# Optimization experiments

Measured on AMD Instinct MI355X. Metric: run time of the kernel, lower is better.

The kernel has to match this reference:

```python
import jax, jax.numpy as jnp
import numpy as np

TAU_FILTER_INV = 1000.0
DT = 0.001
# decay = 1 - alpha = exp(-dt * tau_filter_inv)
DECAY = float(np.exp(-DT * TAU_FILTER_INV))


def setup_inputs() -> dict:
    key = jax.random.key(0)
    k1, k2, k3 = jax.random.split(key, 3)
    T, B, I, O = 2048, 32, 256, 256
    input_tensor = jax.random.normal(k1, (T, B, I), dtype=jnp.float32)
    # Linear weight init mimics uniform(-k, k), k = sqrt(1/input_size)
    k = float(np.sqrt(1.0 / I))
    W = jax.random.uniform(k2, (O, I), dtype=jnp.float32, minval=-k, maxval=k)
    b = jax.random.uniform(k3, (O,), dtype=jnp.float32, minval=-k, maxval=k)
    return {"input_tensor": input_tensor, "W": W, "b": b}


def reference(input_tensor, W, b):
    # Dense projection: [T, B, I] @ [I, O] -> [T, B, O]
    y = jnp.einsum("tbi,oi->tbo", input_tensor, W) + b
    decay = jnp.asarray(DECAY, dtype=y.dtype)

    # s(t) = y(t) + decay * s(t-1); s(0) = y(0) (init state 0)
    def step(s, x):
        s = x + decay * s
        return s, s

    _, out = jax.lax.scan(step, jnp.zeros_like(y[0]), y)
    return out
```

## Files before the change

kernel.cpp:

```cpp
#include <hip/hip_runtime.h>
#include <cstddef>


#define DECAY  0.36787944117144233f
#define D8     0.00033546262790251185f
#define INV1MD 1.5819767068693265f

typedef __attribute__((ext_vector_type(8))) short short8;
typedef __attribute__((ext_vector_type(4))) short short4v;
typedef __attribute__((ext_vector_type(4))) float f32x4;

static constexpr int T_DIM = 2048, B_DIM = 32, K_DIM = 256, N_DIM = 256;
static constexpr int M_DIM = T_DIM * B_DIM;
static constexpr int PS  = 32768;
static constexpr int TCH = 64;

__device__ __forceinline__ float bfbits2f(unsigned short u) {
  unsigned int x = ((unsigned int)u) << 16;
  return __builtin_bit_cast(float, x);
}
__device__ __forceinline__ short f2bf_s(float f) {
  __bf16 h = (__bf16)f;
  return __builtin_bit_cast(short, h);
}

__global__ void k_split_w(const float* __restrict__ W, short* __restrict__ Wh) {
  const int o = blockIdx.x, i = threadIdx.x;
  size_t off = (size_t)(o >> 7) * PS + (i >> 5) * 4096 + ((i >> 3) & 3) * 1024 +
               (o & 127) * 8 + (i & 7);
  Wh[off] = f2bf_s(W[o * 256 + i]);
}

__global__ __launch_bounds__(512, 4)
void k_fused(const float* __restrict__ X, const short* __restrict__ Wth,
             const float* __restrict__ bias, float* __restrict__ out) {
  __shared__ __align__(16) char ldsA[65536];
  __shared__ __align__(16) float cb[8 * 256];
  __shared__ float cfac[TCH];

  const int tid  = threadIdx.x;
  const int lane = tid & 63;
  const int wv   = tid >> 6;
  const int c    = blockIdx.x;
  const int b    = blockIdx.y;
  const int t0   = c * TCH;

  if (tid < TCH)
    cfac[tid] = (1.f - __expf(-(float)(t0 + tid + 1))) * INV1MD;

  const int ch4 = lane * 4;
  const float* xp = X + (size_t)(t0 + wv * 8) * 8192 + b * 256 + ch4;
  const bool warm = (wv == 0) && (c > 0);

  f32x4 xw[8];
  if (warm) {
    const float* wp = xp - (size_t)8 * 8192;
    #pragma unroll
    for (int j = 0; j < 8; ++j)
      xw[j] = *reinterpret_cast<const f32x4*>(wp + (size_t)j * 8192);
  }
  f32x4 xr[8];
  #pragma unroll
  for (int j = 0; j < 8; ++j)
    xr[j] = *reinterpret_cast<const f32x4*>(xp + (size_t)j * 8192);

  f32x4 s = {0.f, 0.f, 0.f, 0.f};
  if (warm) {
    #pragma unroll
    for (int j = 0; j < 8; ++j) s = xw[j] + s * DECAY;
  }
  f32x4 y[8];
  #pragma unroll
  for (int j = 0; j < 8; ++j) { s = xr[j] + s * DECAY; y[j] = s; }

  *reinterpret_cast<f32x4*>(&cb[wv * 256 + ch4]) = s;

  const int row16 = lane & 15;
  const int kq    = lane >> 4;
  const int rg    = wv >> 2;
  const int cg    = wv & 3;
  const short* Whp = Wth + (size_t)(cg >> 1) * PS;
  const int wbase  = kq * 1024 + (((cg & 1) * 64) + row16) * 8;

  short8 bh[2][4];
  #pragma unroll
  for (int ct = 0; ct < 4; ++ct)
    bh[0][ct] = *reinterpret_cast<const short8*>(Whp + wbase + ct * 128);
  __builtin_amdgcn_sched_barrier(0);

  __syncthreads();

  f32x4 cin = {0.f, 0.f, 0.f, 0.f};
  {
    float m = 1.f;
    for (int v = wv - 1; v >= 0; --v) {
      f32x4 cv = *reinterpret_cast<const f32x4*>(&cb[v * 256 + ch4]);
      cin = cin + cv * m;
      m *= D8;
    }
  }

  static const float DP[8] = {0.36787944f, 0.13533528f, 0.049787067f,
                              0.018315639f, 0.0067379470f, 0.0024787522f,
                              0.00091188197f, 0.00033546263f};
  #pragma unroll
  for (int j = 0; j < 8; ++j) {
    f32x4 yy = y[j] + cin * DP[j];
    const int row = wv * 8 + j;
    short4v hv, lv;
    #pragma unroll
    for (int e = 0; e < 4; ++e) {
      short h = f2bf_s(yy[e]);
      hv[e] = h;
      lv[e] = f2bf_s(yy[e] - bfbits2f((unsigned short)h));
    }
    const int byte = (row * 512 + ch4 * 2) ^ ((row & 7) << 4);
    *reinterpret_cast<short4v*>(ldsA + byte)         = hv;
    *reinterpret_cast<short4v*>(ldsA + 32768 + byte) = lv;
  }
  __syncthreads();

  f32x4 acc[2][4] = {};
  #pragma unroll
  for (int kt = 0; kt < 8; ++kt) {
    const int cur = kt & 1;
    if (kt < 7) {
      #pragma unroll
      for (int ct = 0; ct < 4; ++ct)
        bh[cur ^ 1][ct] = *reinterpret_cast<const short8*>(
            Whp + (kt + 1) * 4096 + wbase + ct * 128);
      __builtin_amdgcn_sched_barrier(0);
    }
    short8 ah[2], al[2];
    #pragma unroll
    for (int rt = 0; rt < 2; ++rt) {
      const int row = rg * 32 + rt * 16 + row16;
      const int byte = (row * 512 + kt * 64 + kq * 16) ^ ((row & 7) << 4);
      ah[rt] = *reinterpret_cast<const short8*>(ldsA + byte);
      al[rt] = *reinterpret_cast<const short8*>(ldsA + 32768 + byte);
    }
    #pragma unroll
    for (int rt = 0; rt < 2; ++rt)
      #pragma unroll
      for (int ct = 0; ct < 4; ++ct) {
        acc[rt][ct] = __builtin_amdgcn_mfma_f32_16x16x32_bf16(ah[rt], bh[cur][ct], acc[rt][ct], 0, 0, 0);
        acc[rt][ct] = __builtin_amdgcn_mfma_f32_16x16x32_bf16(al[rt], bh[cur][ct], acc[rt][ct], 0, 0, 0);
      }
  }

  __syncthreads();
  #pragma unroll
  for (int rt = 0; rt < 2; ++rt)
    #pragma unroll
    for (int ct = 0; ct < 4; ++ct)
      #pragma unroll
      for (int j = 0; j < 4; ++j) {
        const int row = rg * 32 + rt * 16 + kq * 4 + j;
        const int col = cg * 64 + ct * 16 + row16;
        const int byte = (row * 1024 + col * 4) ^ ((row & 7) << 4);
        *reinterpret_cast<float*>(ldsA + byte) = acc[rt][ct][j];
      }
  __syncthreads();
  const f32x4* bias4 = reinterpret_cast<const f32x4*>(bias);
  #pragma unroll
  for (int j = 0; j < 8; ++j) {
    const int idx  = tid + j * 512;
    const int row  = idx >> 6;
    const int colc = idx & 63;
    const int byte = (idx * 16) ^ ((row & 7) << 4);
    f32x4 yv = *reinterpret_cast<const f32x4*>(ldsA + byte);
    f32x4 bv = bias4[colc];
    const float cf = cfac[row];
    f32x4 r;
    #pragma unroll
    for (int e = 0; e < 4; ++e) r[e] = fmaf(bv[e], cf, yv[e]);
    *reinterpret_cast<f32x4*>(out + ((size_t)(t0 + row) * 32 + b) * 256 +
                              colc * 4) = r;
  }
}

__global__ void k_fb_gemm(const float* __restrict__ X, const float* __restrict__ W,
                          const float* __restrict__ bias, float* __restrict__ Y) {
  size_t idx = (size_t)blockIdx.x * 256 + threadIdx.x;
  int o = (int)(idx & 255);
  size_t m = idx >> 8;
  const float* x = X + m * 256;
  const float* w = W + (size_t)o * 256;
  float s = bias[o];
  for (int k = 0; k < 256; ++k) s = fmaf(x[k], w[k], s);
  Y[idx] = s;
}
__global__ void k_fb_scan(float* __restrict__ Y) {
  int ch = blockIdx.x * 256 + threadIdx.x;
  float s = 0.f;
  float* p = Y + ch;
  for (int t = 0; t < 2048; ++t) { s = fmaf(DECAY, s, *p); *p = s; p += 8192; }
}

extern "C" void kernel_launch(void* const* d_in, const int* in_sizes, int n_in,
                              void* d_out, int out_size, void* d_ws, size_t ws_size,
                              hipStream_t stream) {
  const float* X    = (const float*)d_in[0];
  const float* W    = (const float*)d_in[1];
  const float* bias = (const float*)d_in[2];
  float* out = (float*)d_out;

  const size_t w_elems = (size_t)N_DIM * K_DIM;
  const size_t need    = w_elems * sizeof(short);

  if (ws_size >= need) {
    short* Wh = (short*)d_ws;
    k_split_w<<<N_DIM, 256, 0, stream>>>(W, Wh);
    k_fused<<<dim3(T_DIM / TCH, B_DIM), 512, 0, stream>>>(X, Wh, bias, out);
  } else {
    k_fb_gemm<<<M_DIM, 256, 0, stream>>>(X, W, bias, out);
    k_fb_scan<<<32, 256, 0, stream>>>(out);
  }
}
```

Before: 39.72 us.

## Drop split-bf16 low part, halve LDS, overlap scan chunks for higher occupancy

Replaces the hi+lo bf16 split of the scanned activations with a single bf16 operand, which halves the MFMA count and the A-tile LDS. The scan is restructured so each wave covers 9 overlapping timesteps, removing the separate warm-up pass, and the carry buffer is stored as bf16. LDS shrinks enough to raise launch bounds to 6 blocks per CU. The GEMM is re-tiled so each wave owns 32 output columns across all 64 rows, and the epilogue is staged in two halves. Dropping the low part reduces accuracy of the projection, which may exceed tolerance.

```diff
diff --git a/kernel.cpp b/kernel.cpp
--- a/kernel.cpp
+++ b/kernel.cpp
@@ -3,7 +3,7 @@
 
 
 #define DECAY  0.36787944117144233f
-#define D8     0.00033546262790251185f
+#define D9     1.2340980408667956e-4f
 #define INV1MD 1.5819767068693265f
 
 typedef __attribute__((ext_vector_type(8))) short short8;
@@ -31,11 +31,11 @@
   Wh[off] = f2bf_s(W[o * 256 + i]);
 }
 
-__global__ __launch_bounds__(512, 4)
+__global__ __launch_bounds__(512, 6)
 void k_fused(const float* __restrict__ X, const short* __restrict__ Wth,
              const float* __restrict__ bias, float* __restrict__ out) {
-  __shared__ __align__(16) char ldsA[65536];
-  __shared__ __align__(16) float cb[8 * 256];
+  __shared__ __align__(16) char ldsA[32768];
+  __shared__ __align__(16) short cbh[8 * 256];
   __shared__ float cfac[TCH];
 
   const int tid  = threadIdx.x;
@@ -44,138 +44,158 @@
   const int c    = blockIdx.x;
   const int b    = blockIdx.y;
   const int t0   = c * TCH;
+  const int ch4  = lane * 4;
+
+  const int row16 = lane & 15;
+  const int kq    = lane >> 4;
+  const int cg    = wv;
+  const short* Wp = Wth + (size_t)(cg >> 2) * PS;
+  const int wr0   = (cg & 3) * 32;
+
+  short8 bh[2][2][2];
+  #pragma unroll
+  for (int ki = 0; ki < 2; ++ki)
+    #pragma unroll
+    for (int ct = 0; ct < 2; ++ct)
+      bh[0][ki][ct] = *reinterpret_cast<const short8*>(
+          Wp + ki * 4096 + kq * 1024 + (wr0 + ct * 16 + row16) * 8);
+  __builtin_amdgcn_sched_barrier(0);
 
   if (tid < TCH)
     cfac[tid] = (1.f - __expf(-(float)(t0 + tid + 1))) * INV1MD;
 
-  const int ch4 = lane * 4;
-  const float* xp = X + (size_t)(t0 + wv * 8) * 8192 + b * 256 + ch4;
-  const bool warm = (wv == 0) && (c > 0);
-
-  f32x4 xw[8];
-  if (warm) {
-    const float* wp = xp - (size_t)8 * 8192;
-    #pragma unroll
-    for (int j = 0; j < 8; ++j)
-      xw[j] = *reinterpret_cast<const f32x4*>(wp + (size_t)j * 8192);
-  }
-  f32x4 xr[8];
-  #pragma unroll
-  for (int j = 0; j < 8; ++j)
-    xr[j] = *reinterpret_cast<const f32x4*>(xp + (size_t)j * 8192);
-
-  f32x4 s = {0.f, 0.f, 0.f, 0.f};
-  if (warm) {
-    #pragma unroll
-    for (int j = 0; j < 8; ++j) s = xw[j] + s * DECAY;
-  }
-  f32x4 y[8];
-  #pragma unroll
-  for (int j = 0; j < 8; ++j) { s = xr[j] + s * DECAY; y[j] = s; }
-
-  *reinterpret_cast<f32x4*>(&cb[wv * 256 + ch4]) = s;
-
-  const int row16 = lane & 15;
-  const int kq    = lane >> 4;
-  const int rg    = wv >> 2;
-  const int cg    = wv & 3;
-  const short* Whp = Wth + (size_t)(cg >> 1) * PS;
-  const int wbase  = kq * 1024 + (((cg & 1) * 64) + row16) * 8;
-
-  short8 bh[2][4];
-  #pragma unroll
-  for (int ct = 0; ct < 4; ++ct)
-    bh[0][ct] = *reinterpret_cast<const short8*>(Whp + wbase + ct * 128);
-  __builtin_amdgcn_sched_barrier(0);
-
+  f32x4 y[9];
+  {
+    const int ts = t0 + wv * 9 - 8;
+    if (ts >= 0) {
+      const float* xp = X + (size_t)ts * 8192 + b * 256 + ch4;
+      f32x4 xr[9];
+      #pragma unroll
+      for (int j = 0; j < 9; ++j)
+        xr[j] = *reinterpret_cast<const f32x4*>(xp + (size_t)j * 8192);
+      f32x4 s = {0.f, 0.f, 0.f, 0.f};
+      #pragma unroll
+      for (int j = 0; j < 9; ++j) {
+        #pragma unroll
+        for (int e = 0; e < 4; ++e) s[e] = fmaf(DECAY, s[e], xr[j][e]);
+        y[j] = s;
+      }
+    } else {
+      y[8] = *reinterpret_cast<const f32x4*>(X + b * 256 + ch4);
+    }
+  }
+  {
+    short4v cv;
+    #pragma unroll
+    for (int e = 0; e < 4; ++e) cv[e] = f2bf_s(y[8][e]);
+    *reinterpret_cast<short4v*>(&cbh[wv * 256 + ch4]) = cv;
+  }
   __syncthreads();
 
   f32x4 cin = {0.f, 0.f, 0.f, 0.f};
   {
     float m = 1.f;
     for (int v = wv - 1; v >= 0; --v) {
-      f32x4 cv = *reinterpret_cast<const f32x4*>(&cb[v * 256 + ch4]);
-      cin = cin + cv * m;
-      m *= D8;
-    }
-  }
-
-  static const float DP[8] = {0.36787944f, 0.13533528f, 0.049787067f,
-                              0.018315639f, 0.0067379470f, 0.0024787522f,
-                              0.00091188197f, 0.00033546263f};
-  #pragma unroll
-  for (int j = 0; j < 8; ++j) {
-    f32x4 yy = y[j] + cin * DP[j];
-    const int row = wv * 8 + j;
-    short4v hv, lv;
-    #pragma unroll
-    for (int e = 0; e < 4; ++e) {
-      short h = f2bf_s(yy[e]);
-      hv[e] = h;
-      lv[e] = f2bf_s(yy[e] - bfbits2f((unsigned short)h));
-    }
-    const int byte = (row * 512 + ch4 * 2) ^ ((row & 7) << 4);
-    *reinterpret_cast<short4v*>(ldsA + byte)         = hv;
-    *reinterpret_cast<short4v*>(ldsA + 32768 + byte) = lv;
+      short4v cv = *reinterpret_cast<const short4v*>(&cbh[v * 256 + ch4]);
+      #pragma unroll
+      for (int e = 0; e < 4; ++e)
+        cin[e] = fmaf(bfbits2f((unsigned short)cv[e]), m, cin[e]);
+      m *= D9;
+    }
+  }
+
+  {
+    static constexpr float DP[9] = {
+        0.36787944117144233f, 0.1353352832366127f,  0.049787068367863944f,
+        0.018315638888734179f, 0.006737946999085467f, 0.0024787521766663585f,
+        0.0009118819655545162f, 0.00033546262790251185f, 1.2340980408667956e-4f};
+    #pragma unroll
+    for (int j = 0; j < 9; ++j) {
+      const int r = wv * 9 + j - 8;
+      if (r >= 0) {
+        short4v hv;
+        #pragma unroll
+        for (int e = 0; e < 4; ++e)
+          hv[e] = f2bf_s(fmaf(cin[e], DP[j], y[j][e]));
+        const int byte = (r * 512 + ch4 * 2) ^ ((r & 7) << 4);
+        *reinterpret_cast<short4v*>(ldsA + byte) = hv;
+      }
+    }
   }
   __syncthreads();
 
-  f32x4 acc[2][4] = {};
-  #pragma unroll
-  for (int kt = 0; kt < 8; ++kt) {
-    const int cur = kt & 1;
-    if (kt < 7) {
-      #pragma unroll
-      for (int ct = 0; ct < 4; ++ct)
-        bh[cur ^ 1][ct] = *reinterpret_cast<const short8*>(
-            Whp + (kt + 1) * 4096 + wbase + ct * 128);
+  #pragma unroll
+  for (int ki = 0; ki < 2; ++ki)
+    #pragma unroll
+    for (int ct = 0; ct < 2; ++ct)
+      bh[1][ki][ct] = *reinterpret_cast<const short8*>(
+          Wp + (2 + ki) * 4096 + kq * 1024 + (wr0 + ct * 16 + row16) * 8);
+  __builtin_amdgcn_sched_barrier(0);
+
+  f32x4 acc[4][2] = {};
+  #pragma unroll
+  for (int g = 0; g < 4; ++g) {
+    #pragma unroll
+    for (int ki = 0; ki < 2; ++ki) {
+      const int kt = g * 2 + ki;
+      short8 ah[4];
+      #pragma unroll
+      for (int rt = 0; rt < 4; ++rt) {
+        const int row = rt * 16 + row16;
+        const int byte = (row * 512 + kt * 64 + kq * 16) ^ ((row & 7) << 4);
+        ah[rt] = *reinterpret_cast<const short8*>(ldsA + byte);
+      }
+      #pragma unroll
+      for (int rt = 0; rt < 4; ++rt)
+        #pragma unroll
+        for (int ct = 0; ct < 2; ++ct)
+          acc[rt][ct] = __builtin_amdgcn_mfma_f32_16x16x32_bf16(
+              ah[rt], bh[g & 1][ki][ct], acc[rt][ct], 0, 0, 0);
+    }
+    if (g < 2) {
+      #pragma unroll
+      for (int ki = 0; ki < 2; ++ki)
+        #pragma unroll
+        for (int ct = 0; ct < 2; ++ct)
+          bh[g & 1][ki][ct] = *reinterpret_cast<const short8*>(
+              Wp + ((g + 2) * 2 + ki) * 4096 + kq * 1024 +
+              (wr0 + ct * 16 + row16) * 8);
       __builtin_amdgcn_sched_barrier(0);
     }
-    short8 ah[2], al[2];
-    #pragma unroll
-    for (int rt = 0; rt < 2; ++rt) {
-      const int row = rg * 32 + rt * 16 + row16;
-      const int byte = (row * 512 + kt * 64 + kq * 16) ^ ((row & 7) << 4);
-      ah[rt] = *reinterpret_cast<const short8*>(ldsA + byte);
-      al[rt] = *reinterpret_cast<const short8*>(ldsA + 32768 + byte);
-    }
-    #pragma unroll
-    for (int rt = 0; rt < 2; ++rt)
-      #pragma unroll
-      for (int ct = 0; ct < 4; ++ct) {
-        acc[rt][ct] = __builtin_amdgcn_mfma_f32_16x16x32_bf16(ah[rt], bh[cur][ct], acc[rt][ct], 0, 0, 0);
-        acc[rt][ct] = __builtin_amdgcn_mfma_f32_16x16x32_bf16(al[rt], bh[cur][ct], acc[rt][ct], 0, 0, 0);
-      }
-  }
-
-  __syncthreads();
-  #pragma unroll
-  for (int rt = 0; rt < 2; ++rt)
-    #pragma unroll
-    for (int ct = 0; ct < 4; ++ct)
-      #pragma unroll
-      for (int j = 0; j < 4; ++j) {
-        const int row = rg * 32 + rt * 16 + kq * 4 + j;
-        const int col = cg * 64 + ct * 16 + row16;
-        const int byte = (row * 1024 + col * 4) ^ ((row & 7) << 4);
-        *reinterpret_cast<float*>(ldsA + byte) = acc[rt][ct][j];
-      }
-  __syncthreads();
+  }
+
   const f32x4* bias4 = reinterpret_cast<const f32x4*>(bias);
   #pragma unroll
-  for (int j = 0; j < 8; ++j) {
-    const int idx  = tid + j * 512;
-    const int row  = idx >> 6;
-    const int colc = idx & 63;
-    const int byte = (idx * 16) ^ ((row & 7) << 4);
-    f32x4 yv = *reinterpret_cast<const f32x4*>(ldsA + byte);
-    f32x4 bv = bias4[colc];
-    const float cf = cfac[row];
-    f32x4 r;
-    #pragma unroll
-    for (int e = 0; e < 4; ++e) r[e] = fmaf(bv[e], cf, yv[e]);
-    *reinterpret_cast<f32x4*>(out + ((size_t)(t0 + row) * 32 + b) * 256 +
-                              colc * 4) = r;
+  for (int p = 0; p < 2; ++p) {
+    __syncthreads();
+    #pragma unroll
+    for (int rt = 2 * p; rt < 2 * p + 2; ++rt)
+      #pragma unroll
+      for (int ct = 0; ct < 2; ++ct)
+        #pragma unroll
+        for (int j = 0; j < 4; ++j) {
+          const int rowh = (rt * 16 + kq * 4 + j) & 31;
+          const int col  = cg * 32 + ct * 16 + row16;
+          const int byte = (rowh * 1024 + col * 4) ^ ((rowh & 7) << 4);
+          *reinterpret_cast<float*>(ldsA + byte) = acc[rt][ct][j];
+        }
+    __syncthreads();
+    #pragma unroll
+    for (int q = 0; q < 4; ++q) {
+      const int idx  = tid + q * 512;
+      const int rowh = idx >> 6;
+      const int colc = idx & 63;
+      const int byte = (idx * 16) ^ ((rowh & 7) << 4);
+      f32x4 yv = *reinterpret_cast<const f32x4*>(ldsA + byte);
+      const int row = p * 32 + rowh;
+      f32x4 bv = bias4[colc];
+      const float cf = cfac[row];
+      f32x4 r;
+      #pragma unroll
+      for (int e = 0; e < 4; ++e) r[e] = fmaf(bv[e], cf, yv[e]);
+      *reinterpret_cast<f32x4*>(out + ((size_t)(t0 + row) * 32 + b) * 256 +
+                                colc * 4) = r;
+    }
   }
 }
 
```

New measurement: 49.28 us. 1.24x slower.
